# Optimization experiments

Hardware: AMD Instinct MI355X
Metric: run time of the kernel (lower is better)

The kernel has to match this reference:

```python
import math
import jax, jax.numpy as jnp
import numpy as np


def _scharr(img):
    # img: (..., H, W) -> (..., 2, H, W); F.conv2d is cross-correlation, as is lax.conv
    kx = jnp.array([[-3., 0., 3.], [10., 0., 10.], [-3., 0., 3.]], jnp.float32)
    k = jnp.stack([kx, kx.T])[:, None]  # (2,1,3,3)
    lead = img.shape[:-2]
    x = img.reshape((-1, 1) + img.shape[-2:])
    y = jax.lax.conv_general_dilated(x, k, (1, 1), 'SAME',
                                     dimension_numbers=('NCHW', 'OIHW', 'NCHW'))
    return y.reshape(lead + (2,) + img.shape[-2:])


def _rotate_nearest(x, angle_deg):
    # torchvision-style rotate with expand=True, nearest interpolation, zero fill
    H, W = x.shape[-2], x.shape[-1]
    a = math.radians(angle_deg)
    c, s = math.cos(a), math.sin(a)
    Hn = int(math.ceil(abs(W * s) + abs(H * c)))
    Wn = int(math.ceil(abs(W * c) + abs(H * s)))
    yy, xx = jnp.meshgrid(jnp.arange(Hn, dtype=jnp.float32),
                          jnp.arange(Wn, dtype=jnp.float32), indexing='ij')
    xg = xx - (Wn - 1) / 2.0
    yg = yy - (Hn - 1) / 2.0
    xi = c * xg - s * yg + (W - 1) / 2.0
    yi = s * xg + c * yg + (H - 1) / 2.0
    xn = jnp.round(xi).astype(jnp.int32)
    yn = jnp.round(yi).astype(jnp.int32)
    valid = (xn >= 0) & (xn < W) & (yn >= 0) & (yn < H)
    out = x[..., jnp.clip(yn, 0, H - 1), jnp.clip(xn, 0, W - 1)]
    return jnp.where(valid, out, jnp.zeros((), x.dtype))


def _gauss_derivs(img):
    # image_gaussian_derivatives: (B, C, H, W) -> (B, C, 8, H, W)
    H, W = img.shape[-2:]
    g = _scharr(img)  # (B, C, 2, H, W)
    # rotated_xywh(H, W, 45) to get crop offsets, exactly as in the source
    a = math.radians(45.0)
    al, be = math.cos(a), math.sin(a)
    cx, cy = W / 2.0, H / 2.0
    pts = [(0., 0.), (W - 1., 0.), (0., H - 1.), (W - 1., H - 1.)]
    rx = [al * px + be * py + (1 - al) * cx - be * cy for px, py in pts]
    ry = [-be * px + al * py + be * cx + (1 - al) * cy for px, py in pts]
    w45 = max(rx) - min(rx)
    h45 = max(ry) - min(ry)
    startx = int(max(0, (w45 - W) / 2))
    starty = int(max(0, (h45 - H) / 2))
    gr = _scharr(_rotate_nearest(img, 45.0))      # (B, C, 2, Hr, Wr)
    grb = _rotate_nearest(gr, -45.0)
    grc = grb[..., starty:starty + H, startx:startx + W]  # (B, C, 2, H, W)
    return jnp.concatenate([jnp.clip(g, 0, None), jnp.clip(g, None, 0),
                            jnp.clip(grc, 0, None), jnp.clip(grc, None, 0)], axis=-3)


def _normalize_min_max(x):
    hmin = x.min(axis=(-2, -1), keepdims=True)
    hmax = x.max(axis=(-2, -1), keepdims=True)
    return (x - hmin) / (hmax - hmin)


def _batched_hist(Z, nbins):
    # Z: (..., N) int in [0, nbins) -> per-row histogram (..., nbins) via one fused segment_sum
    lead = Z.shape[:-1]
    L = int(np.prod(lead))
    Zf = Z.reshape(L, -1)
    ids = (jnp.arange(L, dtype=jnp.int32)[:, None] * nbins + Zf).ravel()
    h = jax.ops.segment_sum(jnp.ones(ids.shape, jnp.float32), ids, num_segments=L * nbins)
    return h.reshape(lead + (nbins,))


def setup_inputs() -> dict:
    key = jax.random.key(0)
    k1, k2 = jax.random.split(key)
    img = jax.random.uniform(k1, (2, 3, 512, 512), jnp.float32)
    reg_lab = jax.random.randint(k2, (2, 1, 3, 512, 512), 0, 256, dtype=jnp.int32)
    return {'img': img, 'reg_lab': reg_lab,
            'color_bins': 25, 'texture_bins': 10, 'num_segments': 256}


def reference(img, reg_lab, color_bins, texture_bins, num_segments):
    B, I, G, H, W = reg_lab.shape
    C = img.shape[1]
    S = num_segments
    # normalized oriented gradient features (B, C, 8, H, W)
    tex = _normalize_min_max(_gauss_derivs(img))
    # region sizes: scatter_add of ones over region labels
    region_sizes = _batched_hist(reg_lab.reshape(B, I, G, H * W), S)  # (B,I,G,S)
    # color histograms
    Zc = (reg_lab[:, :, :, None].astype(jnp.float32) * color_bins
          + img[:, None, None] * (color_bins - 1)).astype(jnp.int32)  # (B,I,G,C,H,W)
    ch = _batched_hist(Zc.reshape(B, I, G, C, H * W), S * color_bins)
    ch = jnp.moveaxis(ch.reshape(B, I, G, C, S, color_bins), -2, -3)  # (B,I,G,S,C,cb)
    ch = ch / ch.sum(axis=(-2, -1), keepdims=True)
    # texture histograms
    Zt = (reg_lab[:, :, :, None, None].astype(jnp.float32) * texture_bins
          + tex[:, None, None] * (texture_bins - 1)).astype(jnp.int32)  # (B,I,G,C,8,H,W)
    th = _batched_hist(Zt.reshape(B, I, G, C, 8, H * W), S * texture_bins)
    th = jnp.moveaxis(th.reshape(B, I, G, C, 8, S, texture_bins), -2, -4)  # (B,I,G,S,C,8,tb)
    th = th / th.sum(axis=(-3, -2, -1), keepdims=True)
    # per-region bounding boxes via segment min/max (replaces the 5-deep python loop)
    grid_y, grid_x = jnp.meshgrid(jnp.arange(H, dtype=jnp.int32),
                                  jnp.arange(W, dtype=jnp.int32), indexing='ij')
    BIG = B * I * G
    ids = (jnp.arange(BIG, dtype=jnp.int32)[:, None] * S
           + reg_lab.reshape(BIG, H * W)).ravel()
    xs = jnp.tile(grid_x.ravel(), BIG)
    ys = jnp.tile(grid_y.ravel(), BIG)
    n = BIG * S
    xmin = jax.ops.segment_min(xs, ids, num_segments=n)
    xmax = jax.ops.segment_max(xs, ids, num_segments=n)
    ymin = jax.ops.segment_min(ys, ids, num_segments=n)
    ymax = jax.ops.segment_max(ys, ids, num_segments=n)
    nonempty = region_sizes.reshape(n) > 0
    xmin = jnp.where(nonempty, xmin, W)
    ymin = jnp.where(nonempty, ymin, H)
    xmax = jnp.where(nonempty, xmax, 0)
    ymax = jnp.where(nonempty, ymax, 0)
    xywh = jnp.stack([xmin, ymin, xmax - xmin, ymax - ymin], axis=-1).reshape(B, I, G, S, 4)
    return region_sizes, ch, th, xywh
```

## Files before the change

### kernel.cpp

```cpp
#include <hip/hip_runtime.h>
#include <climits>

#define HW 262144
#define IW 512
#define RN 725
#define NSEG 256
#define CH_OFF 1536
#define TH_OFF 116736
#define XY_OFF 485376
#define NBLK 256
#define THP 24
#define CHP 32

#define ASTR 67
#define RSTR 73
#define ROFF 156

static __device__ __forceinline__ float rtap_l(const float* __restrict__ Rt,
                                               int rx0, int ry0, int cx, int cy) {
    if (cx < 0 || cx >= RN || cy < 0 || cy >= RN) return 0.f;
    const float cs = 0.7071067811865476f;
    float xg = (float)cx - 362.0f;
    float yg = (float)cy - 362.0f;
    float xi = cs * xg - cs * yg + 255.5f;
    float yi = cs * xg + cs * yg + 255.5f;
    int xs = (int)rintf(xi);
    int ys = (int)rintf(yi);
    if (xs < 0 || xs >= IW || ys < 0 || ys >= IW) return 0.f;
    return Rt[(ys - ry0) * RSTR + (xs - rx0)];
}

static __device__ __forceinline__ void mm_of_map(const float* __restrict__ pmin,
                                                 const float* __restrict__ pmax,
                                                 int m, float* slo, float* shi,
                                                 float& mn, float& mx) {
    int tid = threadIdx.x;
    float lo = 3.4e38f, hi = -3.4e38f;
    for (int i = tid; i < NBLK; i += 256) {
        lo = fminf(lo, pmin[m * NBLK + i]);
        hi = fmaxf(hi, pmax[m * NBLK + i]);
    }
    slo[tid] = lo; shi[tid] = hi;
    __syncthreads();
    for (int off = 128; off > 0; off >>= 1) {
        if (tid < off) {
            slo[tid] = fminf(slo[tid], slo[tid + off]);
            shi[tid] = fmaxf(shi[tid], shi[tid + off]);
        }
        __syncthreads();
    }
    mn = slo[0]; mx = shi[0];
    __syncthreads();
}

__global__ __launch_bounds__(256) void k_grad(
    const float* __restrict__ img, const int* __restrict__ lab,
    float* __restrict__ gmaps,
    float* __restrict__ pmin, float* __restrict__ pmax,
    float* __restrict__ out, int* __restrict__ bbmin, int* __restrict__ bbmax,
    unsigned char* __restrict__ lab8)
{
    int t = blockIdx.x;
    int bc = blockIdx.y;
    int tid = threadIdx.x;
    if (bc == 0 && t < 6) {
        out[t * 256 + tid] = 0.0f;
    } else if (bc == 1 && t < 12) {
        int i = t * 256 + tid;
        bbmin[i] = INT_MAX;
        bbmax[i] = INT_MIN;
    }
    {
        int i = t * 256 + tid;
        int4 l = ((const int4*)(lab + (size_t)bc * HW))[i];
        unsigned v = (unsigned)(l.x & 255) | ((unsigned)(l.y & 255) << 8) |
                     ((unsigned)(l.z & 255) << 16) | ((unsigned)(l.w & 255) << 24);
        ((unsigned*)(lab8 + (size_t)bc * HW))[i] = v;
    }
    __shared__ float At[18 * ASTR];
    __shared__ float Rt[24 * RSTR];
    __shared__ float slo[4][256], shi[4][256];
    int tx0 = (t & 7) << 6;
    int ty0 = (t >> 3) << 4;
    const float* im = img + (size_t)bc * HW;
    int lane = tid & 63, wr = tid >> 6;
    for (int r = wr; r < 18; r += 4) {
        int gy = ty0 - 1 + r;
        bool yok = (gy >= 0 && gy < IW);
        int gx = tx0 - 1 + lane;
        At[r * ASTR + lane] = (yok && gx >= 0 && gx < IW) ? im[gy * IW + gx] : 0.f;
        if (lane < 2) {
            int gx2 = gx + 64;
            At[r * ASTR + lane + 64] = (yok && gx2 >= 0 && gx2 < IW) ? im[gy * IW + gx2] : 0.f;
        }
    }
    for (int r = wr; r < 24; r += 4) {
        int gy = ty0 - ROFF + r;
        bool yok = (gy >= 0 && gy < IW);
        int gx = tx0 - ROFF + lane;
        Rt[r * RSTR + lane] = (yok && gx >= 0 && gx < IW) ? im[gy * IW + gx] : 0.f;
        if (lane < 8) {
            int gx2 = gx + 64;
            Rt[r * RSTR + lane + 64] = (yok && gx2 >= 0 && gx2 < IW) ? im[gy * IW + gx2] : 0.f;
        }
    }
    __syncthreads();
    const float cs = 0.7071067811865476f;
    int rx0 = tx0 - ROFF, ry0 = ty0 - ROFF;
    float mn0 = 3.4e38f, mx0 = -3.4e38f, mn1 = 3.4e38f, mx1 = -3.4e38f;
    float mn2 = 3.4e38f, mx2 = -3.4e38f, mn3 = 3.4e38f, mx3 = -3.4e38f;
    #pragma unroll
    for (int it = 0; it < 4; ++it) {
        int ly = wr * 4 + it;
        int x = tx0 + lane, y = ty0 + ly;
        int p = y * IW + x;
        const float* Ar = At + ly * ASTR + lane;
        float a  = Ar[0],            b2 = Ar[1],            c2 = Ar[2];
        float d2 = Ar[ASTR],                                 e2 = Ar[ASTR + 2];
        float f2 = Ar[2 * ASTR],     h2 = Ar[2 * ASTR + 1], i9 = Ar[2 * ASTR + 2];
        float g0 = -3.f*a + 3.f*c2 + 10.f*d2 + 10.f*e2 - 3.f*f2 + 3.f*i9;
        float g1 = -3.f*a + 10.f*b2 - 3.f*c2 + 3.f*f2 + 10.f*h2 + 3.f*i9;
        gmaps[((size_t)(bc*2+0))*HW + p] = g0;
        gmaps[((size_t)(bc*2+1))*HW + p] = g1;
        float xgc = (float)(x + 105) - 512.5f;
        float ygc = (float)(y + 105) - 512.5f;
        float t1 = cs * xgc, t2 = cs * ygc;
        float xi = (t1 + t2) + 362.0f;
        float yi = (-t1 + t2) + 362.0f;
        int xn = (int)rintf(xi);
        int yn = (int)rintf(yi);
        float r0 = 0.f, r1 = 0.f;
        if (xn >= 0 && xn < RN && yn >= 0 && yn < RN) {
            float ra = rtap_l(Rt, rx0, ry0, xn-1, yn-1);
            float rb = rtap_l(Rt, rx0, ry0, xn,   yn-1);
            float rc = rtap_l(Rt, rx0, ry0, xn+1, yn-1);
            float rd = rtap_l(Rt, rx0, ry0, xn-1, yn);
            float re = rtap_l(Rt, rx0, ry0, xn+1, yn);
            float rf = rtap_l(Rt, rx0, ry0, xn-1, yn+1);
            float rh = rtap_l(Rt, rx0, ry0, xn,   yn+1);
            float ri = rtap_l(Rt, rx0, ry0, xn+1, yn+1);
            r0 = -3.f*ra + 3.f*rc + 10.f*rd + 10.f*re - 3.f*rf + 3.f*ri;
            r1 = -3.f*ra + 10.f*rb - 3.f*rc + 3.f*rf + 10.f*rh + 3.f*ri;
        }
        gmaps[((size_t)(12 + bc*2+0))*HW + p] = r0;
        gmaps[((size_t)(12 + bc*2+1))*HW + p] = r1;
        mn0 = fminf(mn0, g0); mx0 = fmaxf(mx0, g0);
        mn1 = fminf(mn1, g1); mx1 = fmaxf(mx1, g1);
        mn2 = fminf(mn2, r0); mx2 = fmaxf(mx2, r0);
        mn3 = fminf(mn3, r1); mx3 = fmaxf(mx3, r1);
    }
    slo[0][tid] = mn0; shi[0][tid] = mx0;
    slo[1][tid] = mn1; shi[1][tid] = mx1;
    slo[2][tid] = mn2; shi[2][tid] = mx2;
    slo[3][tid] = mn3; shi[3][tid] = mx3;
    __syncthreads();
    for (int off = 128; off > 0; off >>= 1) {
        if (tid < off) {
            #pragma unroll
            for (int k = 0; k < 4; ++k) {
                slo[k][tid] = fminf(slo[k][tid], slo[k][tid + off]);
                shi[k][tid] = fmaxf(shi[k][tid], shi[k][tid + off]);
            }
        }
        __syncthreads();
    }
    if (tid < 4) {
        int m = (tid < 2) ? (bc*2 + tid) : (12 + bc*2 + (tid - 2));
        pmin[m * NBLK + t] = slo[tid][0];
        pmax[m * NBLK + t] = shi[tid][0];
    }
}

__global__ __launch_bounds__(256) void k_regchist(
    const float* __restrict__ img, const unsigned char* __restrict__ lab8,
    float* __restrict__ rs_out, int* __restrict__ bbmin, int* __restrict__ bbmax,
    unsigned* __restrict__ chp)
{
    __shared__ unsigned cnt[NSEG * 25];
    __shared__ unsigned rcnt[NSEG];
    __shared__ int sxmin[NSEG], sxmax[NSEG], symin[NSEG], symax[NSEG];
    int gy = blockIdx.y;
    int c = gy % 3;
    int bg = gy / 3;
    int b = bg / 3;
    int tid = threadIdx.x;
    bool do_reg = (c == 0);
    for (int i = tid; i < NSEG * 25; i += 256) cnt[i] = 0;
    if (do_reg) {
        rcnt[tid] = 0; sxmin[tid] = INT_MAX; sxmax[tid] = INT_MIN;
        symin[tid] = INT_MAX; symax[tid] = INT_MIN;
    }
    __syncthreads();
    const float4* ip = (const float4*)(img + ((size_t)b * 3 + c) * HW);
    const unsigned* lp = (const unsigned*)(lab8 + (size_t)bg * HW);
    int stride = 256 * gridDim.x;
    for (int i = blockIdx.x * 256 + tid; i < HW / 4; i += stride) {
        float4 v4 = ip[i];
        unsigned l4 = lp[i];
        int l0 = l4 & 255, l1 = (l4 >> 8) & 255, l2 = (l4 >> 16) & 255, l3 = l4 >> 24;
        int b0 = (int)((float)l0 * 25.0f + v4.x * 24.0f);
        int b1 = (int)((float)l1 * 25.0f + v4.y * 24.0f);
        int b2 = (int)((float)l2 * 25.0f + v4.z * 24.0f);
        int b3 = (int)((float)l3 * 25.0f + v4.w * 24.0f);
        b0 = min(max(b0, 0), 6399); b1 = min(max(b1, 0), 6399);
        b2 = min(max(b2, 0), 6399); b3 = min(max(b3, 0), 6399);
        atomicAdd(&cnt[b0], 1u); atomicAdd(&cnt[b1], 1u);
        atomicAdd(&cnt[b2], 1u); atomicAdd(&cnt[b3], 1u);
        if (do_reg) {
            int p = i << 2;
            int y = p >> 9, x = p & 511;
            atomicAdd(&rcnt[l0], 1u); atomicAdd(&rcnt[l1], 1u);
            atomicAdd(&rcnt[l2], 1u); atomicAdd(&rcnt[l3], 1u);
            atomicMin(&sxmin[l0], x);     atomicMax(&sxmax[l0], x);
            atomicMin(&sxmin[l1], x + 1); atomicMax(&sxmax[l1], x + 1);
            atomicMin(&sxmin[l2], x + 2); atomicMax(&sxmax[l2], x + 2);
            atomicMin(&sxmin[l3], x + 3); atomicMax(&sxmax[l3], x + 3);
            atomicMin(&symin[l0], y); atomicMax(&symax[l0], y);
            atomicMin(&symin[l1], y); atomicMax(&symax[l1], y);
            atomicMin(&symin[l2], y); atomicMax(&symax[l2], y);
            atomicMin(&symin[l3], y); atomicMax(&symax[l3], y);
        }
    }
    __syncthreads();
    unsigned* dst = chp + ((size_t)gy * CHP + blockIdx.x) * 6400;
    for (int i = tid; i < NSEG * 25; i += 256) dst[i] = cnt[i];
    if (do_reg) {
        if (rcnt[tid]) atomicAdd(&rs_out[bg * NSEG + tid], (float)rcnt[tid]);
        if (sxmin[tid] != INT_MAX) {
            atomicMin(&bbmin[bg * NSEG + tid], sxmin[tid]);
            atomicMax(&bbmax[bg * NSEG + tid], sxmax[tid]);
            atomicMin(&bbmin[1536 + bg * NSEG + tid], symin[tid]);
            atomicMax(&bbmax[1536 + bg * NSEG + tid], symax[tid]);
        }
    }
}

__global__ __launch_bounds__(256) void k_thist(
    const float* __restrict__ maps, const unsigned char* __restrict__ lab8,
    const float* __restrict__ pmin, const float* __restrict__ pmax,
    unsigned* __restrict__ thp)
{
    __shared__ unsigned cnt[5120];
    __shared__ float slo[256], shi[256];
    int gy = blockIdx.y;
    int split = blockIdx.x;
    int gi = gy % 3;
    int r = gy / 3;
    int base = r & 1;
    int bd = r >> 1;
    int d = bd & 1;
    int bc = bd >> 1;
    int b = bc / 3;
    int m = base * 12 + bc * 2 + d;
    float mn, mx;
    mm_of_map(pmin, pmax, m, slo, shi, mn, mx);
    for (int i = threadIdx.x; i < 5120; i += 256) cnt[i] = 0;
    __syncthreads();
    float hminp = fmaxf(mn, 0.f), denp = fmaxf(mx, 0.f) - hminp;
    float hminn = fminf(mn, 0.f), denn = fminf(mx, 0.f) - hminn;
    const float4* src = (const float4*)(maps + (size_t)m * HW);
    const unsigned* lp = (const unsigned*)(lab8 + (size_t)(b * 3 + gi) * HW);
    for (int i = split * 256 + threadIdx.x; i < HW / 4; i += 256 * THP) {
        float4 v4 = src[i];
        unsigned l4 = lp[i];
#define TH1(V, SH)                                                     \
        {                                                              \
            float v = (V);                                             \
            bool ge = (v >= 0.f);                                      \
            float hm = ge ? hminp : hminn;                             \
            float dn = ge ? denp : denn;                               \
            float t9 = ((v - hm) / dn) * 9.0f;                         \
            int bi = (int)((float)((l4 >> SH) & 255u) * 10.0f + t9);   \
            bi = min(max(bi, 0), 2559);                                \
            atomicAdd(&cnt[(ge ? 0 : 2560) + bi], 1u);                 \
        }
        TH1(v4.x, 0) TH1(v4.y, 8) TH1(v4.z, 16) TH1(v4.w, 24)
#undef TH1
    }
    __syncthreads();
    unsigned* dst = thp + ((size_t)(gy * THP + split)) * 5120;
    for (int i = threadIdx.x; i < 5120; i += 256) dst[i] = cnt[i];
}

__global__ __launch_bounds__(256) void k_thfinal(
    const unsigned* __restrict__ thp, const unsigned* __restrict__ chp,
    const float* __restrict__ pmin, const float* __restrict__ pmax,
    const int* __restrict__ bbmin, const int* __restrict__ bbmax,
    float* __restrict__ out)
{
    int tid = threadIdx.x;
    int bx = blockIdx.x;
    if (bx < 288) {
        __shared__ unsigned hist[1280];
        __shared__ float slo[256], shi[256];
        int gy = bx >> 2;
        int ck = bx & 3;
        int l0 = ck << 6;
        int gi = gy % 3; int r = gy / 3; int base = r & 1;
        int bd = r >> 1; int d = bd & 1; int bc = bd >> 1;
        int b = bc / 3, c = bc - b * 3;
        int m = base * 12 + bc * 2 + d;
        float mn, mx;
        mm_of_map(pmin, pmax, m, slo, shi, mn, mx);
        int g0off = l0 * 10;
        for (int i = tid; i < 1280; i += 256) {
            int g = (i < 640) ? (g0off + i) : (2560 + g0off + (i - 640));
            unsigned s = 0;
            #pragma unroll 4
            for (int p = 0; p < THP; ++p) s += thp[((size_t)(gy * THP + p)) * 5120 + g];
            hist[i] = s;
        }
        __syncthreads();
        if (tid < 64) {
            int l = l0 + tid;
            unsigned nge = 0;
            for (int tb = 0; tb < 10; ++tb) nge += hist[tid * 10 + tb];
            float rsf = out[(b * 3 + gi) * NSEG + l];
            unsigned rsu = (unsigned)rsf;
            unsigned nlt = (rsu >= nge) ? (rsu - nge) : 0u;
            float hminp = fmaxf(mn, 0.f), denp = fmaxf(mx, 0.f) - hminp;
            float hminn = fminf(mn, 0.f), denn = fminf(mx, 0.f) - hminn;
            float la = (float)l;
            float tp0 = ((0.0f - hminp) / denp) * 9.0f;
            float tn0 = ((0.0f - hminn) / denn) * 9.0f;
            int bp = (int)(la * 10.0f + tp0); bp = min(max(bp, 0), 2559);
            int bn = (int)(la * 10.0f + tn0); bn = min(max(bn, 0), 2559);
            if (nlt && bp >= g0off && bp < g0off + 640) atomicAdd(&hist[bp - g0off], nlt);
            if (nge && bn >= g0off && bn < g0off + 640) atomicAdd(&hist[640 + bn - g0off], nge);
        }
        __syncthreads();
        for (int i = tid; i < 1280; i += 256) {
            int pos = (i < 640);
            int rr = pos ? i : i - 640;
            int seg = l0 + rr / 10, tb = rr % 10;
            int tt = base * 4 + (pos ? 0 : 2) + d;
            float rsf = out[(b * 3 + gi) * NSEG + seg];
            out[TH_OFF + ((size_t)((b * 3 + gi) * NSEG + seg) * 3 + c) * 80 + tt * 10 + tb] =
                (float)hist[i] / (24.0f * rsf);
        }
    } else {
        for (int seg = bx - 288; seg < 1536; seg += (gridDim.x - 288)) {
            int bg = seg >> 8;
            int s = seg & 255;
            float rsf = out[seg];
            float cd = 3.0f * rsf;
            float* ch = out + CH_OFF + (size_t)seg * 75;
            for (int i = tid; i < 75; i += 256) {
                int c = i / 25, cb = i - c * 25;
                unsigned sum = 0;
                const unsigned* src = chp + ((size_t)(bg * 3 + c) * CHP) * 6400 + s * 25 + cb;
                #pragma unroll 4
                for (int p = 0; p < CHP; ++p) sum += src[(size_t)p * 6400];
                ch[i] = (float)sum / cd;
            }
            if (tid == 0) {
                int xmin, xmax, ymin, ymax;
                if (rsf > 0.f) {
                    xmin = bbmin[seg]; ymin = bbmin[1536 + seg];
                    xmax = bbmax[seg]; ymax = bbmax[1536 + seg];
                } else {
                    xmin = IW; ymin = IW; xmax = 0; ymax = 0;
                }
                float* xy = out + XY_OFF + (size_t)seg * 4;
                xy[0] = (float)xmin; xy[1] = (float)ymin;
                xy[2] = (float)(xmax - xmin); xy[3] = (float)(ymax - ymin);
            }
        }
    }
}

extern "C" void kernel_launch(void* const* d_in, const int* in_sizes, int n_in,
                              void* d_out, int out_size, void* d_ws, size_t ws_size,
                              hipStream_t stream) {
    const float* img = (const float*)d_in[0];
    const int* lab = (const int*)d_in[1];
    float* out = (float*)d_out;

    float* gmaps = (float*)d_ws;
    float* pmin = gmaps + (size_t)24 * HW;
    float* pmax = pmin + 24 * NBLK;
    int* bbmin = (int*)(pmax + 24 * NBLK);
    int* bbmax = bbmin + 3072;
    unsigned* thp = (unsigned*)(bbmax + 3072);
    unsigned* chp = thp + (size_t)72 * THP * 5120;
    unsigned char* lab8 = (unsigned char*)(chp + (size_t)18 * CHP * 6400);

    hipLaunchKernelGGL(k_grad, dim3(NBLK, 6), dim3(256), 0, stream,
                       img, lab, gmaps, pmin, pmax, out, bbmin, bbmax, lab8);
    hipLaunchKernelGGL(k_regchist, dim3(CHP, 18), dim3(256), 0, stream,
                       img, lab8, out, bbmin, bbmax, chp);
    hipLaunchKernelGGL(k_thist, dim3(THP, 72), dim3(256), 0, stream, gmaps, lab8, pmin, pmax, thp);
    hipLaunchKernelGGL(k_thfinal, dim3(288 + 256), dim3(256), 0, stream, thp, chp, pmin, pmax, bbmin, bbmax, out);
}
```

Baseline: 131.8 us.

## Merge gradient and color/region histogram kernels into one interleaved front kernel

Combines the gradient kernel and the region/color-histogram kernel into a single launch whose even blocks compute gradients and odd blocks compute histograms, reading int labels directly instead of waiting for the packed byte labels. Region counts and bounding boxes now go to per-block partial buffers that the final kernel reduces, which removes the global atomics and the zero-init pass. The color-histogram split factor is doubled. This drops one launch and a serial dependency, at the cost of more partial-buffer traffic and more reduction work in the final kernel.

Measured after the change: 246.0 us. 86.7% more time.

```diff
diff --git a/kernel.cpp b/kernel.cpp
--- a/kernel.cpp
+++ b/kernel.cpp
@@ -10,7 +10,8 @@
 #define XY_OFF 485376
 #define NBLK 256
 #define THP 24
-#define CHP 32
+#define CHP 64
+#define RSP 64
 
 #define ASTR 67
 #define RSTR 73
@@ -53,184 +54,183 @@
     __syncthreads();
 }
 
-__global__ __launch_bounds__(256) void k_grad(
+__global__ __launch_bounds__(256) void k_front(
     const float* __restrict__ img, const int* __restrict__ lab,
-    float* __restrict__ gmaps,
-    float* __restrict__ pmin, float* __restrict__ pmax,
-    float* __restrict__ out, int* __restrict__ bbmin, int* __restrict__ bbmax,
-    unsigned char* __restrict__ lab8)
+    float* __restrict__ gmaps, float* __restrict__ pmin, float* __restrict__ pmax,
+    unsigned char* __restrict__ lab8, unsigned* __restrict__ chp,
+    unsigned* __restrict__ rsp, int* __restrict__ bxmin, int* __restrict__ bxmax,
+    int* __restrict__ bymin, int* __restrict__ bymax)
 {
-    int t = blockIdx.x;
-    int bc = blockIdx.y;
+    __shared__ __align__(16) unsigned char smem[25600];
+    int bxid = blockIdx.x;
     int tid = threadIdx.x;
-    if (bc == 0 && t < 6) {
-        out[t * 256 + tid] = 0.0f;
-    } else if (bc == 1 && t < 12) {
-        int i = t * 256 + tid;
-        bbmin[i] = INT_MAX;
-        bbmax[i] = INT_MIN;
-    }
-    {
-        int i = t * 256 + tid;
-        int4 l = ((const int4*)(lab + (size_t)bc * HW))[i];
-        unsigned v = (unsigned)(l.x & 255) | ((unsigned)(l.y & 255) << 8) |
-                     ((unsigned)(l.z & 255) << 16) | ((unsigned)(l.w & 255) << 24);
-        ((unsigned*)(lab8 + (size_t)bc * HW))[i] = v;
-    }
-    __shared__ float At[18 * ASTR];
-    __shared__ float Rt[24 * RSTR];
-    __shared__ float slo[4][256], shi[4][256];
-    int tx0 = (t & 7) << 6;
-    int ty0 = (t >> 3) << 4;
-    const float* im = img + (size_t)bc * HW;
-    int lane = tid & 63, wr = tid >> 6;
-    for (int r = wr; r < 18; r += 4) {
-        int gy = ty0 - 1 + r;
-        bool yok = (gy >= 0 && gy < IW);
-        int gx = tx0 - 1 + lane;
-        At[r * ASTR + lane] = (yok && gx >= 0 && gx < IW) ? im[gy * IW + gx] : 0.f;
-        if (lane < 2) {
-            int gx2 = gx + 64;
-            At[r * ASTR + lane + 64] = (yok && gx2 >= 0 && gx2 < IW) ? im[gy * IW + gx2] : 0.f;
-        }
-    }
-    for (int r = wr; r < 24; r += 4) {
-        int gy = ty0 - ROFF + r;
-        bool yok = (gy >= 0 && gy < IW);
-        int gx = tx0 - ROFF + lane;
-        Rt[r * RSTR + lane] = (yok && gx >= 0 && gx < IW) ? im[gy * IW + gx] : 0.f;
-        if (lane < 8) {
-            int gx2 = gx + 64;
-            Rt[r * RSTR + lane + 64] = (yok && gx2 >= 0 && gx2 < IW) ? im[gy * IW + gx2] : 0.f;
-        }
-    }
-    __syncthreads();
-    const float cs = 0.7071067811865476f;
-    int rx0 = tx0 - ROFF, ry0 = ty0 - ROFF;
-    float mn0 = 3.4e38f, mx0 = -3.4e38f, mn1 = 3.4e38f, mx1 = -3.4e38f;
-    float mn2 = 3.4e38f, mx2 = -3.4e38f, mn3 = 3.4e38f, mx3 = -3.4e38f;
-    #pragma unroll
-    for (int it = 0; it < 4; ++it) {
-        int ly = wr * 4 + it;
-        int x = tx0 + lane, y = ty0 + ly;
-        int p = y * IW + x;
-        const float* Ar = At + ly * ASTR + lane;
-        float a  = Ar[0],            b2 = Ar[1],            c2 = Ar[2];
-        float d2 = Ar[ASTR],                                 e2 = Ar[ASTR + 2];
-        float f2 = Ar[2 * ASTR],     h2 = Ar[2 * ASTR + 1], i9 = Ar[2 * ASTR + 2];
-        float g0 = -3.f*a + 3.f*c2 + 10.f*d2 + 10.f*e2 - 3.f*f2 + 3.f*i9;
-        float g1 = -3.f*a + 10.f*b2 - 3.f*c2 + 3.f*f2 + 10.f*h2 + 3.f*i9;
-        gmaps[((size_t)(bc*2+0))*HW + p] = g0;
-        gmaps[((size_t)(bc*2+1))*HW + p] = g1;
-        float xgc = (float)(x + 105) - 512.5f;
-        float ygc = (float)(y + 105) - 512.5f;
-        float t1 = cs * xgc, t2 = cs * ygc;
-        float xi = (t1 + t2) + 362.0f;
-        float yi = (-t1 + t2) + 362.0f;
-        int xn = (int)rintf(xi);
-        int yn = (int)rintf(yi);
-        float r0 = 0.f, r1 = 0.f;
-        if (xn >= 0 && xn < RN && yn >= 0 && yn < RN) {
-            float ra = rtap_l(Rt, rx0, ry0, xn-1, yn-1);
-            float rb = rtap_l(Rt, rx0, ry0, xn,   yn-1);
-            float rc = rtap_l(Rt, rx0, ry0, xn+1, yn-1);
-            float rd = rtap_l(Rt, rx0, ry0, xn-1, yn);
-            float re = rtap_l(Rt, rx0, ry0, xn+1, yn);
-            float rf = rtap_l(Rt, rx0, ry0, xn-1, yn+1);
-            float rh = rtap_l(Rt, rx0, ry0, xn,   yn+1);
-            float ri = rtap_l(Rt, rx0, ry0, xn+1, yn+1);
-            r0 = -3.f*ra + 3.f*rc + 10.f*rd + 10.f*re - 3.f*rf + 3.f*ri;
-            r1 = -3.f*ra + 10.f*rb - 3.f*rc + 3.f*rf + 10.f*rh + 3.f*ri;
-        }
-        gmaps[((size_t)(12 + bc*2+0))*HW + p] = r0;
-        gmaps[((size_t)(12 + bc*2+1))*HW + p] = r1;
-        mn0 = fminf(mn0, g0); mx0 = fmaxf(mx0, g0);
-        mn1 = fminf(mn1, g1); mx1 = fmaxf(mx1, g1);
-        mn2 = fminf(mn2, r0); mx2 = fmaxf(mx2, r0);
-        mn3 = fminf(mn3, r1); mx3 = fmaxf(mx3, r1);
-    }
-    slo[0][tid] = mn0; shi[0][tid] = mx0;
-    slo[1][tid] = mn1; shi[1][tid] = mx1;
-    slo[2][tid] = mn2; shi[2][tid] = mx2;
-    slo[3][tid] = mn3; shi[3][tid] = mx3;
-    __syncthreads();
-    for (int off = 128; off > 0; off >>= 1) {
-        if (tid < off) {
-            #pragma unroll
-            for (int k = 0; k < 4; ++k) {
-                slo[k][tid] = fminf(slo[k][tid], slo[k][tid + off]);
-                shi[k][tid] = fmaxf(shi[k][tid], shi[k][tid + off]);
+    if ((bxid & 1) == 0) {
+        int u = bxid >> 1;
+        int tile = u & 255;
+        int bc = u >> 8;
+        float* At = (float*)smem;
+        float* Rt = At + 18 * ASTR;
+        float (*slo)[256] = (float (*)[256])(Rt + 24 * RSTR);
+        float (*shi)[256] = slo + 4;
+        {
+            int i = tile * 256 + tid;
+            int4 l = ((const int4*)(lab + (size_t)bc * HW))[i];
+            unsigned v = (unsigned)(l.x & 255) | ((unsigned)(l.y & 255) << 8) |
+                         ((unsigned)(l.z & 255) << 16) | ((unsigned)(l.w & 255) << 24);
+            ((unsigned*)(lab8 + (size_t)bc * HW))[i] = v;
+        }
+        int tx0 = (tile & 7) << 6;
+        int ty0 = (tile >> 3) << 4;
+        const float* im = img + (size_t)bc * HW;
+        int lane = tid & 63, wr = tid >> 6;
+        for (int r = wr; r < 18; r += 4) {
+            int gy = ty0 - 1 + r;
+            bool yok = (gy >= 0 && gy < IW);
+            int gx = tx0 - 1 + lane;
+            At[r * ASTR + lane] = (yok && gx >= 0 && gx < IW) ? im[gy * IW + gx] : 0.f;
+            if (lane < 2) {
+                int gx2 = gx + 64;
+                At[r * ASTR + lane + 64] = (yok && gx2 >= 0 && gx2 < IW) ? im[gy * IW + gx2] : 0.f;
+            }
+        }
+        for (int r = wr; r < 24; r += 4) {
+            int gy = ty0 - ROFF + r;
+            bool yok = (gy >= 0 && gy < IW);
+            int gx = tx0 - ROFF + lane;
+            Rt[r * RSTR + lane] = (yok && gx >= 0 && gx < IW) ? im[gy * IW + gx] : 0.f;
+            if (lane < 8) {
+                int gx2 = gx + 64;
+                Rt[r * RSTR + lane + 64] = (yok && gx2 >= 0 && gx2 < IW) ? im[gy * IW + gx2] : 0.f;
             }
         }
         __syncthreads();
-    }
-    if (tid < 4) {
-        int m = (tid < 2) ? (bc*2 + tid) : (12 + bc*2 + (tid - 2));
-        pmin[m * NBLK + t] = slo[tid][0];
-        pmax[m * NBLK + t] = shi[tid][0];
-    }
-}
-
-__global__ __launch_bounds__(256) void k_regchist(
-    const float* __restrict__ img, const unsigned char* __restrict__ lab8,
-    float* __restrict__ rs_out, int* __restrict__ bbmin, int* __restrict__ bbmax,
-    unsigned* __restrict__ chp)
-{
-    __shared__ unsigned cnt[NSEG * 25];
-    __shared__ unsigned rcnt[NSEG];
-    __shared__ int sxmin[NSEG], sxmax[NSEG], symin[NSEG], symax[NSEG];
-    int gy = blockIdx.y;
-    int c = gy % 3;
-    int bg = gy / 3;
-    int b = bg / 3;
-    int tid = threadIdx.x;
-    bool do_reg = (c == 0);
-    for (int i = tid; i < NSEG * 25; i += 256) cnt[i] = 0;
-    if (do_reg) {
-        rcnt[tid] = 0; sxmin[tid] = INT_MAX; sxmax[tid] = INT_MIN;
-        symin[tid] = INT_MAX; symax[tid] = INT_MIN;
-    }
-    __syncthreads();
-    const float4* ip = (const float4*)(img + ((size_t)b * 3 + c) * HW);
-    const unsigned* lp = (const unsigned*)(lab8 + (size_t)bg * HW);
-    int stride = 256 * gridDim.x;
-    for (int i = blockIdx.x * 256 + tid; i < HW / 4; i += stride) {
-        float4 v4 = ip[i];
-        unsigned l4 = lp[i];
-        int l0 = l4 & 255, l1 = (l4 >> 8) & 255, l2 = (l4 >> 16) & 255, l3 = l4 >> 24;
-        int b0 = (int)((float)l0 * 25.0f + v4.x * 24.0f);
-        int b1 = (int)((float)l1 * 25.0f + v4.y * 24.0f);
-        int b2 = (int)((float)l2 * 25.0f + v4.z * 24.0f);
-        int b3 = (int)((float)l3 * 25.0f + v4.w * 24.0f);
-        b0 = min(max(b0, 0), 6399); b1 = min(max(b1, 0), 6399);
-        b2 = min(max(b2, 0), 6399); b3 = min(max(b3, 0), 6399);
-        atomicAdd(&cnt[b0], 1u); atomicAdd(&cnt[b1], 1u);
-        atomicAdd(&cnt[b2], 1u); atomicAdd(&cnt[b3], 1u);
-        if (do_reg) {
-            int p = i << 2;
-            int y = p >> 9, x = p & 511;
-            atomicAdd(&rcnt[l0], 1u); atomicAdd(&rcnt[l1], 1u);
-            atomicAdd(&rcnt[l2], 1u); atomicAdd(&rcnt[l3], 1u);
-            atomicMin(&sxmin[l0], x);     atomicMax(&sxmax[l0], x);
-            atomicMin(&sxmin[l1], x + 1); atomicMax(&sxmax[l1], x + 1);
-            atomicMin(&sxmin[l2], x + 2); atomicMax(&sxmax[l2], x + 2);
-            atomicMin(&sxmin[l3], x + 3); atomicMax(&sxmax[l3], x + 3);
-            atomicMin(&symin[l0], y); atomicMax(&symax[l0], y);
-            atomicMin(&symin[l1], y); atomicMax(&symax[l1], y);
-            atomicMin(&symin[l2], y); atomicMax(&symax[l2], y);
-            atomicMin(&symin[l3], y); atomicMax(&symax[l3], y);
-        }
-    }
-    __syncthreads();
-    unsigned* dst = chp + ((size_t)gy * CHP + blockIdx.x) * 6400;
-    for (int i = tid; i < NSEG * 25; i += 256) dst[i] = cnt[i];
-    if (do_reg) {
-        if (rcnt[tid]) atomicAdd(&rs_out[bg * NSEG + tid], (float)rcnt[tid]);
-        if (sxmin[tid] != INT_MAX) {
-            atomicMin(&bbmin[bg * NSEG + tid], sxmin[tid]);
-            atomicMax(&bbmax[bg * NSEG + tid], sxmax[tid]);
-            atomicMin(&bbmin[1536 + bg * NSEG + tid], symin[tid]);
-            atomicMax(&bbmax[1536 + bg * NSEG + tid], symax[tid]);
+        const float cs = 0.7071067811865476f;
+        int rx0 = tx0 - ROFF, ry0 = ty0 - ROFF;
+        float mn0 = 3.4e38f, mx0 = -3.4e38f, mn1 = 3.4e38f, mx1 = -3.4e38f;
+        float mn2 = 3.4e38f, mx2 = -3.4e38f, mn3 = 3.4e38f, mx3 = -3.4e38f;
+        #pragma unroll
+        for (int it = 0; it < 4; ++it) {
+            int ly = wr * 4 + it;
+            int x = tx0 + lane, y = ty0 + ly;
+            int p = y * IW + x;
+            const float* Ar = At + ly * ASTR + lane;
+            float a  = Ar[0],            b2 = Ar[1],            c2 = Ar[2];
+            float d2 = Ar[ASTR],                                 e2 = Ar[ASTR + 2];
+            float f2 = Ar[2 * ASTR],     h2 = Ar[2 * ASTR + 1], i9 = Ar[2 * ASTR + 2];
+            float g0 = -3.f*a + 3.f*c2 + 10.f*d2 + 10.f*e2 - 3.f*f2 + 3.f*i9;
+            float g1 = -3.f*a + 10.f*b2 - 3.f*c2 + 3.f*f2 + 10.f*h2 + 3.f*i9;
+            gmaps[((size_t)(bc*2+0))*HW + p] = g0;
+            gmaps[((size_t)(bc*2+1))*HW + p] = g1;
+            float xgc = (float)(x + 105) - 512.5f;
+            float ygc = (float)(y + 105) - 512.5f;
+            float t1 = cs * xgc, t2 = cs * ygc;
+            float xi = (t1 + t2) + 362.0f;
+            float yi = (-t1 + t2) + 362.0f;
+            int xn = (int)rintf(xi);
+            int yn = (int)rintf(yi);
+            float r0 = 0.f, r1 = 0.f;
+            if (xn >= 0 && xn < RN && yn >= 0 && yn < RN) {
+                float ra = rtap_l(Rt, rx0, ry0, xn-1, yn-1);
+                float rb = rtap_l(Rt, rx0, ry0, xn,   yn-1);
+                float rc = rtap_l(Rt, rx0, ry0, xn+1, yn-1);
+                float rd = rtap_l(Rt, rx0, ry0, xn-1, yn);
+                float re = rtap_l(Rt, rx0, ry0, xn+1, yn);
+                float rf = rtap_l(Rt, rx0, ry0, xn-1, yn+1);
+                float rh = rtap_l(Rt, rx0, ry0, xn,   yn+1);
+                float ri = rtap_l(Rt, rx0, ry0, xn+1, yn+1);
+                r0 = -3.f*ra + 3.f*rc + 10.f*rd + 10.f*re - 3.f*rf + 3.f*ri;
+                r1 = -3.f*ra + 10.f*rb - 3.f*rc + 3.f*rf + 10.f*rh + 3.f*ri;
+            }
+            gmaps[((size_t)(12 + bc*2+0))*HW + p] = r0;
+            gmaps[((size_t)(12 + bc*2+1))*HW + p] = r1;
+            mn0 = fminf(mn0, g0); mx0 = fmaxf(mx0, g0);
+            mn1 = fminf(mn1, g1); mx1 = fmaxf(mx1, g1);
+            mn2 = fminf(mn2, r0); mx2 = fmaxf(mx2, r0);
+            mn3 = fminf(mn3, r1); mx3 = fmaxf(mx3, r1);
+        }
+        slo[0][tid] = mn0; shi[0][tid] = mx0;
+        slo[1][tid] = mn1; shi[1][tid] = mx1;
+        slo[2][tid] = mn2; shi[2][tid] = mx2;
+        slo[3][tid] = mn3; shi[3][tid] = mx3;
+        __syncthreads();
+        for (int off = 128; off > 0; off >>= 1) {
+            if (tid < off) {
+                #pragma unroll
+                for (int k = 0; k < 4; ++k) {
+                    slo[k][tid] = fminf(slo[k][tid], slo[k][tid + off]);
+                    shi[k][tid] = fmaxf(shi[k][tid], shi[k][tid + off]);
+                }
+            }
+            __syncthreads();
+        }
+        if (tid < 4) {
+            int m = (tid < 2) ? (bc*2 + tid) : (12 + bc*2 + (tid - 2));
+            pmin[m * NBLK + tile] = slo[tid][0];
+            pmax[m * NBLK + tile] = shi[tid][0];
+        }
+    } else {
+        int v = bxid >> 1;
+        if (v < 18 * CHP) {
+            int gy = v / CHP;
+            int sp = v - gy * CHP;
+            int c = gy % 3;
+            int bg = gy / 3;
+            int b = bg / 3;
+            unsigned* cnt = (unsigned*)smem;
+            for (int i = tid; i < NSEG * 25; i += 256) cnt[i] = 0;
+            __syncthreads();
+            const float4* ip = (const float4*)(img + ((size_t)b * 3 + c) * HW);
+            const int4* lp = (const int4*)(lab + (size_t)bg * HW);
+            for (int i = sp * 256 + tid; i < HW / 4; i += 256 * CHP) {
+                float4 v4 = ip[i];
+                int4 l4 = lp[i];
+                int l0 = l4.x & 255, l1 = l4.y & 255, l2 = l4.z & 255, l3 = l4.w & 255;
+                int b0 = (int)((float)l0 * 25.0f + v4.x * 24.0f);
+                int b1 = (int)((float)l1 * 25.0f + v4.y * 24.0f);
+                int b2 = (int)((float)l2 * 25.0f + v4.z * 24.0f);
+                int b3 = (int)((float)l3 * 25.0f + v4.w * 24.0f);
+                b0 = min(max(b0, 0), 6399); b1 = min(max(b1, 0), 6399);
+                b2 = min(max(b2, 0), 6399); b3 = min(max(b3, 0), 6399);
+                atomicAdd(&cnt[b0], 1u); atomicAdd(&cnt[b1], 1u);
+                atomicAdd(&cnt[b2], 1u); atomicAdd(&cnt[b3], 1u);
+            }
+            __syncthreads();
+            unsigned* dst = chp + ((size_t)gy * CHP + sp) * 6400;
+            for (int i = tid; i < NSEG * 25; i += 256) dst[i] = cnt[i];
+        } else {
+            int w = v - 18 * CHP;
+            int bg = w / RSP;
+            int sp = w - bg * RSP;
+            unsigned* rcnt = (unsigned*)smem;
+            int* sxmin = (int*)(rcnt + NSEG);
+            int* sxmax = sxmin + NSEG;
+            int* symin = sxmax + NSEG;
+            int* symax = symin + NSEG;
+            rcnt[tid] = 0; sxmin[tid] = INT_MAX; sxmax[tid] = INT_MIN;
+            symin[tid] = INT_MAX; symax[tid] = INT_MIN;
+            __syncthreads();
+            const int4* lp = (const int4*)(lab + (size_t)bg * HW);
+            for (int i = sp * 256 + tid; i < HW / 4; i += 256 * RSP) {
+                int4 l4 = lp[i];
+                int l0 = l4.x & 255, l1 = l4.y & 255, l2 = l4.z & 255, l3 = l4.w & 255;
+                int p = i << 2;
+                int y = p >> 9, x = p & 511;
+                atomicAdd(&rcnt[l0], 1u); atomicAdd(&rcnt[l1], 1u);
+                atomicAdd(&rcnt[l2], 1u); atomicAdd(&rcnt[l3], 1u);
+                atomicMin(&sxmin[l0], x);     atomicMax(&sxmax[l0], x);
+                atomicMin(&sxmin[l1], x + 1); atomicMax(&sxmax[l1], x + 1);
+                atomicMin(&sxmin[l2], x + 2); atomicMax(&sxmax[l2], x + 2);
+                atomicMin(&sxmin[l3], x + 3); atomicMax(&sxmax[l3], x + 3);
+                atomicMin(&symin[l0], y); atomicMax(&symax[l0], y);
+                atomicMin(&symin[l1], y); atomicMax(&symax[l1], y);
+                atomicMin(&symin[l2], y); atomicMax(&symax[l2], y);
+                atomicMin(&symin[l3], y); atomicMax(&symax[l3], y);
+            }
+            __syncthreads();
+            size_t pi = (size_t)(bg * RSP + sp) * NSEG + tid;
+            rsp[pi] = rcnt[tid];
+            bxmin[pi] = sxmin[tid]; bxmax[pi] = sxmax[tid];
+            bymin[pi] = symin[tid]; bymax[pi] = symax[tid];
         }
     }
 }
@@ -284,14 +284,17 @@
 
 __global__ __launch_bounds__(256) void k_thfinal(
     const unsigned* __restrict__ thp, const unsigned* __restrict__ chp,
+    const unsigned* __restrict__ rsp,
     const float* __restrict__ pmin, const float* __restrict__ pmax,
-    const int* __restrict__ bbmin, const int* __restrict__ bbmax,
+    const int* __restrict__ bxmin, const int* __restrict__ bxmax,
+    const int* __restrict__ bymin, const int* __restrict__ bymax,
     float* __restrict__ out)
 {
     int tid = threadIdx.x;
     int bx = blockIdx.x;
     if (bx < 288) {
         __shared__ unsigned hist[1280];
+        __shared__ unsigned srs[64];
         __shared__ float slo[256], shi[256];
         int gy = bx >> 2;
         int ck = bx & 3;
@@ -300,6 +303,7 @@
         int bd = r >> 1; int d = bd & 1; int bc = bd >> 1;
         int b = bc / 3, c = bc - b * 3;
         int m = base * 12 + bc * 2 + d;
+        int bg = b * 3 + gi;
         float mn, mx;
         mm_of_map(pmin, pmax, m, slo, shi, mn, mx);
         int g0off = l0 * 10;
@@ -310,13 +314,18 @@
             for (int p = 0; p < THP; ++p) s += thp[((size_t)(gy * THP + p)) * 5120 + g];
             hist[i] = s;
         }
+        if (tid < 64) {
+            unsigned s = 0;
+            #pragma unroll 4
+            for (int p = 0; p < RSP; ++p) s += rsp[((size_t)(bg * RSP + p)) * NSEG + l0 + tid];
+            srs[tid] = s;
+        }
         __syncthreads();
         if (tid < 64) {
             int l = l0 + tid;
             unsigned nge = 0;
             for (int tb = 0; tb < 10; ++tb) nge += hist[tid * 10 + tb];
-            float rsf = out[(b * 3 + gi) * NSEG + l];
-            unsigned rsu = (unsigned)rsf;
+            unsigned rsu = srs[tid];
             unsigned nlt = (rsu >= nge) ? (rsu - nge) : 0u;
             float hminp = fmaxf(mn, 0.f), denp = fmaxf(mx, 0.f) - hminp;
             float hminn = fminf(mn, 0.f), denn = fminf(mx, 0.f) - hminn;
@@ -332,38 +341,47 @@
         for (int i = tid; i < 1280; i += 256) {
             int pos = (i < 640);
             int rr = pos ? i : i - 640;
-            int seg = l0 + rr / 10, tb = rr % 10;
+            int lseg = rr / 10, tb = rr % 10;
+            int seg = l0 + lseg;
             int tt = base * 4 + (pos ? 0 : 2) + d;
-            float rsf = out[(b * 3 + gi) * NSEG + seg];
-            out[TH_OFF + ((size_t)((b * 3 + gi) * NSEG + seg) * 3 + c) * 80 + tt * 10 + tb] =
+            float rsf = (float)srs[lseg];
+            out[TH_OFF + ((size_t)(bg * NSEG + seg) * 3 + c) * 80 + tt * 10 + tb] =
                 (float)hist[i] / (24.0f * rsf);
         }
     } else {
         for (int seg = bx - 288; seg < 1536; seg += (gridDim.x - 288)) {
             int bg = seg >> 8;
             int s = seg & 255;
-            float rsf = out[seg];
-            float cd = 3.0f * rsf;
-            float* ch = out + CH_OFF + (size_t)seg * 75;
-            for (int i = tid; i < 75; i += 256) {
-                int c = i / 25, cb = i - c * 25;
-                unsigned sum = 0;
-                const unsigned* src = chp + ((size_t)(bg * 3 + c) * CHP) * 6400 + s * 25 + cb;
+            if (tid < 76) {
+                unsigned rs = 0;
+                const unsigned* rp = rsp + (size_t)(bg * RSP) * NSEG + s;
                 #pragma unroll 4
-                for (int p = 0; p < CHP; ++p) sum += src[(size_t)p * 6400];
-                ch[i] = (float)sum / cd;
-            }
-            if (tid == 0) {
-                int xmin, xmax, ymin, ymax;
-                if (rsf > 0.f) {
-                    xmin = bbmin[seg]; ymin = bbmin[1536 + seg];
-                    xmax = bbmax[seg]; ymax = bbmax[1536 + seg];
+                for (int p = 0; p < RSP; ++p) rs += rp[(size_t)p * NSEG];
+                float rsf = (float)rs;
+                if (tid < 75) {
+                    int c = tid / 25, cb = tid - c * 25;
+                    float cd = 3.0f * rsf;
+                    const unsigned* src = chp + ((size_t)((bg * 3 + c) * CHP)) * 6400 + s * 25 + cb;
+                    unsigned sum = 0;
+                    #pragma unroll 4
+                    for (int p = 0; p < CHP; ++p) sum += src[(size_t)p * 6400];
+                    out[CH_OFF + (size_t)seg * 75 + tid] = (float)sum / cd;
                 } else {
-                    xmin = IW; ymin = IW; xmax = 0; ymax = 0;
+                    out[seg] = rsf;
+                    int xmn = INT_MAX, xmx = INT_MIN, ymn = INT_MAX, ymx = INT_MIN;
+                    const int* p0 = bxmin + (size_t)(bg * RSP) * NSEG + s;
+                    const int* p1 = bxmax + (size_t)(bg * RSP) * NSEG + s;
+                    const int* p2 = bymin + (size_t)(bg * RSP) * NSEG + s;
+                    const int* p3 = bymax + (size_t)(bg * RSP) * NSEG + s;
+                    for (int p = 0; p < RSP; ++p) {
+                        xmn = min(xmn, p0[(size_t)p * NSEG]); xmx = max(xmx, p1[(size_t)p * NSEG]);
+                        ymn = min(ymn, p2[(size_t)p * NSEG]); ymx = max(ymx, p3[(size_t)p * NSEG]);
+                    }
+                    if (!(rsf > 0.f)) { xmn = IW; ymn = IW; xmx = 0; ymx = 0; }
+                    float* xy = out + XY_OFF + (size_t)seg * 4;
+                    xy[0] = (float)xmn; xy[1] = (float)ymn;
+                    xy[2] = (float)(xmx - xmn); xy[3] = (float)(ymx - ymn);
                 }
-                float* xy = out + XY_OFF + (size_t)seg * 4;
-                xy[0] = (float)xmin; xy[1] = (float)ymin;
-                xy[2] = (float)(xmax - xmin); xy[3] = (float)(ymax - ymin);
             }
         }
     }
@@ -379,16 +397,18 @@
     float* gmaps = (float*)d_ws;
     float* pmin = gmaps + (size_t)24 * HW;
     float* pmax = pmin + 24 * NBLK;
-    int* bbmin = (int*)(pmax + 24 * NBLK);
-    int* bbmax = bbmin + 3072;
-    unsigned* thp = (unsigned*)(bbmax + 3072);
+    unsigned* thp = (unsigned*)(pmax + 24 * NBLK);
     unsigned* chp = thp + (size_t)72 * THP * 5120;
     unsigned char* lab8 = (unsigned char*)(chp + (size_t)18 * CHP * 6400);
-
-    hipLaunchKernelGGL(k_grad, dim3(NBLK, 6), dim3(256), 0, stream,
-                       img, lab, gmaps, pmin, pmax, out, bbmin, bbmax, lab8);
-    hipLaunchKernelGGL(k_regchist, dim3(CHP, 18), dim3(256), 0, stream,
-                       img, lab8, out, bbmin, bbmax, chp);
+    unsigned* rsp = (unsigned*)(lab8 + (size_t)6 * HW);
+    int* bxmin = (int*)(rsp + 6 * RSP * NSEG);
+    int* bxmax = bxmin + 6 * RSP * NSEG;
+    int* bymin = bxmax + 6 * RSP * NSEG;
+    int* bymax = bymin + 6 * RSP * NSEG;
+
+    hipLaunchKernelGGL(k_front, dim3(3072), dim3(256), 0, stream,
+                       img, lab, gmaps, pmin, pmax, lab8, chp, rsp, bxmin, bxmax, bymin, bymax);
     hipLaunchKernelGGL(k_thist, dim3(THP, 72), dim3(256), 0, stream, gmaps, lab8, pmin, pmax, thp);
-    hipLaunchKernelGGL(k_thfinal, dim3(288 + 256), dim3(256), 0, stream, thp, chp, pmin, pmax, bbmin, bbmax, out);
-}
+    hipLaunchKernelGGL(k_thfinal, dim3(288 + 256), dim3(256), 0, stream,
+                       thp, chp, rsp, pmin, pmax, bxmin, bxmax, bymin, bymax, out);
+}
```
